# Optimization experiments

Measured on AMD Instinct MI355X. Metric: run time of the kernel, lower is better.

The kernel has to match this reference:

```python
import jax, jax.numpy as jnp
import numpy as np

TEMPERATURE = 0.07
MARGIN = 0.2
EPS = 1e-8  # matches torch F.cosine_similarity eps


def _cosine_matrix(a, b):
    # a: (N, D), b: (M, D) -> (N, M) pairwise cosine similarity
    an = a / jnp.clip(jnp.linalg.norm(a, axis=-1, keepdims=True), EPS)
    bn = b / jnp.clip(jnp.linalg.norm(b, axis=-1, keepdims=True), EPS)
    return an @ bn.T


def setup_inputs() -> dict:
    key = jax.random.key(0)
    k1, k2, k3 = jax.random.split(key, 3)
    return {
        "step_embeddings": jax.random.normal(k1, (8192, 1024), dtype=jnp.float32),
        "modal_embeddings": jax.random.normal(k2, (4096, 1024), dtype=jnp.float32),
        "negative_modal_embeddings": jax.random.normal(k3, (4096, 1024), dtype=jnp.float32),
    }


def reference(step_embeddings, modal_embeddings, negative_modal_embeddings):
    # --- step-modal alignment (max cosine sim per step, averaged) ---
    S = _cosine_matrix(step_embeddings, modal_embeddings)        # (N, M)
    per_step = S.max(axis=1)                                      # (N,)
    alignment = per_step.mean()

    # --- attention-weighted alignment (use_attention=True) ---
    logits = (step_embeddings @ modal_embeddings.T) / TEMPERATURE  # (N, M)
    attention = jax.nn.softmax(logits, axis=1)
    weighted_alignment = (S * attention).sum(axis=1).mean()

    # --- contrastive coherence against negatives ---
    Sn = _cosine_matrix(step_embeddings, negative_modal_embeddings)
    negative_alignment = Sn.max(axis=1).mean()
    positive_alignment = alignment
    contrastive_score = positive_alignment - negative_alignment
    margin_score = jax.nn.relu(contrastive_score - MARGIN)

    # --- per-step coherence (same max-cosine per step) ---
    min_step_coherence = per_step.min()

    # overall uses weighted_alignment (attention on), mixed with contrastive
    overall = 0.7 * weighted_alignment + 0.3 * contrastive_score

    return (alignment, weighted_alignment, attention, contrastive_score,
            margin_score, positive_alignment, negative_alignment,
            per_step, min_step_coherence, overall)
```

## Files before the change

### kernel.cpp

```cpp
#include <hip/hip_runtime.h>
#include <cmath>


#define WAVE 64

typedef __bf16 bf16x8_t __attribute__((ext_vector_type(8)));
typedef __bf16 bf16x4_t __attribute__((ext_vector_type(4)));
typedef float f32x4_t __attribute__((ext_vector_type(4)));

__device__ __forceinline__ float wave_reduce_sum(float v) {
#pragma unroll
    for (int o = 32; o > 0; o >>= 1) v += __shfl_down(v, o, WAVE);
    return v;
}
__device__ __forceinline__ float wave_reduce_max(float v) {
#pragma unroll
    for (int o = 32; o > 0; o >>= 1) v = fmaxf(v, __shfl_down(v, o, WAVE));
    return v;
}
__device__ __forceinline__ float wave_reduce_min(float v) {
#pragma unroll
    for (int o = 32; o > 0; o >>= 1) v = fminf(v, __shfl_down(v, o, WAVE));
    return v;
}

__device__ __forceinline__ unsigned enc_f(float f) {
    unsigned u = __float_as_uint(f);
    return (u & 0x80000000u) ? ~u : (u | 0x80000000u);
}
__device__ __forceinline__ float dec_f(unsigned e) {
    unsigned u = (e & 0x80000000u) ? (e & 0x7fffffffu) : ~e;
    return __uint_as_float(u);
}

__global__ __launch_bounds__(256)
void convert_norms_kernel(const float* __restrict__ step,
                          const float* __restrict__ modal,
                          const float* __restrict__ negs,
                          char* __restrict__ arena,
                          float* __restrict__ ina, float* __restrict__ inb,
                          float* __restrict__ inn,
                          unsigned* __restrict__ negmax_u, int N, int M) {
    const int tid = threadIdx.x, lane = tid & 63, wv = tid >> 6;
    const int b = blockIdx.x * 4 + wv;
    const float* src;
    if (b < N)          src = step  + (size_t)b * 1024;
    else if (b < N + M) src = modal + (size_t)(b - N) * 1024;
    else                src = negs  + (size_t)(b - N - M) * 1024;

    char* cb = arena + (((size_t)(b >> 2)) << 14) + ((size_t)(b & 3) << 11) + 8192;
    float s = 0.0f;
#pragma unroll
    for (int q = 0; q < 4; q++) {
        const int idx = lane + q * 64;
        const float4 v = ((const float4*)src)[idx];
        bf16x4_t o;
        o[0] = (__bf16)v.x; o[1] = (__bf16)v.y;
        o[2] = (__bf16)v.z; o[3] = (__bf16)v.w;
        *(bf16x4_t*)(cb + (size_t)idx * 8) = o;
        s += v.x * v.x + v.y * v.y + v.z * v.z + v.w * v.w;
    }
    s = wave_reduce_sum(s);
    if (lane == 0) {
        const float inv = 1.0f / fmaxf(sqrtf(s), 1e-8f);
        if (b < N)          { ina[b] = inv; negmax_u[b] = 0u; }
        else if (b < N + M) inb[b - N] = inv;
        else                inn[b - N - M] = inv;
    }
}

#define GLD16(g, l)                                                        \
    __builtin_amdgcn_global_load_lds(                                     \
        (const __attribute__((address_space(1))) void*)(g),               \
        (__attribute__((address_space(3))) void*)(l), 16, 0, 0)

#define PIPE_BARRIER() asm volatile(                                       \
    "s_waitcnt vmcnt(0) lgkmcnt(0)\n\ts_barrier" ::: "memory")

__global__ __launch_bounds__(256, 2)
void gemm_fused_kernel(char* __restrict__ arena, int N, int M,
                       const float* __restrict__ inv_nn,
                       unsigned* __restrict__ negmax_u) {
    __shared__ __bf16 As[2][128 * 64];
    __shared__ __bf16 Bs[2][128 * 64];

    const int lin = blockIdx.x;
    const int st  = lin >> 7;
    const int r128 = lin & 127;
    const int bxi = (st & 7) * 8 + (r128 & 7);
    const int byi = (st >> 3) * 16 + (r128 >> 3);
    const int bm = byi * 128, bn = bxi * 128;

    const int t = threadIdx.x, w = t >> 6, lane = t & 63;
    const int lane16 = lane & 15, lq = lane >> 4;
    const int wm = (w & 1) * 64, wn = (w >> 1) * 64;

    const int s_is_b  = w >> 1;
    const int rowbase = (w & 1) * 64;
    const int ln3 = lane >> 3;
    const int q_g = (lane & 7) ^ ln3;
    const int cbase = (s_is_b ? (N + bn) : bm) + rowbase;
    const int cc = cbase + ln3;
    const size_t off0 = (((size_t)(cc >> 2)) << 14) +
                        ((size_t)(cc & 3) << 11) + 8192 + (size_t)q_g * 16;
    const char* gbase = arena + off0;
    const int ldsoff = rowbase * 64;
    __bf16* ldsw0 = (s_is_b ? Bs[0] : As[0]) + ldsoff;
    __bf16* ldsw1 = (s_is_b ? Bs[1] : As[1]) + ldsoff;

    f32x4_t acc[4][4];
#pragma unroll
    for (int i = 0; i < 4; i++)
#pragma unroll
        for (int j = 0; j < 4; j++) acc[i][j] = (f32x4_t){0.f, 0.f, 0.f, 0.f};

    const int sxr = lane16 & 7;

#pragma unroll
    for (int r = 0; r < 8; r++)
        GLD16(gbase + (size_t)r * 32768, ldsw0 + r * 512);

    for (int it = 0; it < 16; ++it) {
        PIPE_BARRIER();
        const int cur = it & 1;

        bf16x8_t af[2][4], bf[2][4];
#pragma unroll
        for (int kk = 0; kk < 2; kk++) {
            const int qo = ((lq + kk * 4) ^ sxr) * 8;
#pragma unroll
            for (int i = 0; i < 4; i++)
                af[kk][i] = *(const bf16x8_t*)&As[cur][(wm + i * 16 + lane16) * 64 + qo];
#pragma unroll
            for (int j = 0; j < 4; j++)
                bf[kk][j] = *(const bf16x8_t*)&Bs[cur][(wn + j * 16 + lane16) * 64 + qo];
        }

        if (it + 1 < 16) {
            const size_t k0b = (size_t)(it + 1) * 128;
            __bf16* ldsw = cur ? ldsw0 : ldsw1;
#pragma unroll
            for (int r = 0; r < 8; r++)
                GLD16(gbase + (size_t)r * 32768 + k0b, ldsw + r * 512);
        }

#pragma unroll
        for (int kk = 0; kk < 2; kk++)
#pragma unroll
            for (int i = 0; i < 4; i++)
#pragma unroll
                for (int j = 0; j < 4; j++)
                    acc[i][j] = __builtin_amdgcn_mfma_f32_16x16x32_bf16(
                        af[kk][i], bf[kk][j], acc[i][j], 0, 0, 0);
    }

    if (bn < M) {
#pragma unroll
        for (int i = 0; i < 4; i++) {
#pragma unroll
            for (int r = 0; r < 4; r++) {
                const int grow = bm + wm + i * 16 + lq * 4 + r;
                __bf16* dst = (__bf16*)(arena + ((size_t)grow << 14)) +
                              bn + wn + lane16;
#pragma unroll
                for (int j = 0; j < 4; j++)
                    dst[j * 16] = (__bf16)acc[i][j][r];
            }
        }
    } else {
        float invn[4];
#pragma unroll
        for (int j = 0; j < 4; j++)
            invn[j] = inv_nn[(bn - M) + wn + j * 16 + lane16];
#pragma unroll
        for (int i = 0; i < 4; i++) {
#pragma unroll
            for (int r = 0; r < 4; r++) {
                float v = acc[i][0][r] * invn[0];
                v = fmaxf(v, acc[i][1][r] * invn[1]);
                v = fmaxf(v, acc[i][2][r] * invn[2]);
                v = fmaxf(v, acc[i][3][r] * invn[3]);
#pragma unroll
                for (int o = 8; o > 0; o >>= 1)
                    v = fmaxf(v, __shfl_xor(v, o, WAVE));
                if (lane16 == 0)
                    atomicMax(&negmax_u[bm + wm + i * 16 + lq * 4 + r], enc_f(v));
            }
        }
    }
}

#define CUT 2.0f
#define MAXCAND 64

__global__ __launch_bounds__(256)
void softmax_fix_kernel(char* __restrict__ arena, const float* __restrict__ step,
                        const float* __restrict__ modal,
                        const float* __restrict__ ina, const float* __restrict__ inb,
                        float* __restrict__ perstep, float* __restrict__ wout,
                        float* __restrict__ attn) {
    const int row = blockIdx.x, tid = threadIdx.x;
    const int lane = tid & 63, wv = tid >> 6;

    __shared__ float srow_s[1024];
    __shared__ float red[8];
    __shared__ float bcast[2];
    __shared__ int   cand[MAXCAND];
    __shared__ float exact[MAXCAND];
    __shared__ int   cnt;

    if (tid == 0) cnt = 0;
    ((float4*)srow_s)[tid] = ((const float4*)(step + (size_t)row * 1024))[tid];

    const __bf16* gb = (const __bf16*)(arena + ((size_t)row << 14));
    float vals[16];
    float invn[16];
#pragma unroll
    for (int g = 0; g < 4; g++) {
        const bf16x4_t v = *(const bf16x4_t*)(gb + g * 1024 + tid * 4);
        const float4 x = *(const float4*)(inb + g * 1024 + tid * 4);
        vals[g * 4 + 0] = (float)v[0]; vals[g * 4 + 1] = (float)v[1];
        vals[g * 4 + 2] = (float)v[2]; vals[g * 4 + 3] = (float)v[3];
        invn[g * 4 + 0] = x.x; invn[g * 4 + 1] = x.y;
        invn[g * 4 + 2] = x.z; invn[g * 4 + 3] = x.w;
    }

    float dmax = -3.4e38f;
#pragma unroll
    for (int j = 0; j < 16; j++) dmax = fmaxf(dmax, vals[j]);
    float wm = wave_reduce_max(dmax);
    if (lane == 0) red[wv] = wm;
    __syncthreads();
    if (tid == 0) bcast[0] = fmaxf(fmaxf(red[0], red[1]), fmaxf(red[2], red[3]));
    __syncthreads();
    const float m0 = bcast[0];

    const float thr = m0 - CUT;
#pragma unroll
    for (int g = 0; g < 4; g++)
#pragma unroll
        for (int u = 0; u < 4; u++) {
            if (vals[g * 4 + u] >= thr) {
                const int pos = atomicAdd(&cnt, 1);
                if (pos < MAXCAND) cand[pos] = g * 1024 + tid * 4 + u;
            }
        }
    __syncthreads();
    const int nc = min(cnt, MAXCAND);

    for (int i = wv; i < nc; i += 4) {
        const float* mrow = modal + (size_t)cand[i] * 1024;
        float p = 0.0f;
#pragma unroll
        for (int q = 0; q < 16; q++) {
            const int idx = lane + q * 64;
            p = fmaf(srow_s[idx], mrow[idx], p);
        }
        p = wave_reduce_sum(p);
        if (lane == 0) exact[i] = p;
    }
    __syncthreads();

    for (int i = 0; i < nc; i++) {
        const int c = cand[i];
        if (((c & 1023) >> 2) == tid) vals[(c >> 10) * 4 + (c & 3)] = exact[i];
    }

    float dmax2 = -3.4e38f, cmax = -3.4e38f;
#pragma unroll
    for (int j = 0; j < 16; j++) {
        dmax2 = fmaxf(dmax2, vals[j]);
        cmax = fmaxf(cmax, vals[j] * invn[j]);
    }
    float wg = wave_reduce_max(dmax2);
    float wc = wave_reduce_max(cmax);
    if (lane == 0) { red[wv] = wg; red[4 + wv] = wc; }
    __syncthreads();
    if (tid == 0) {
        bcast[0] = fmaxf(fmaxf(red[0], red[1]), fmaxf(red[2], red[3]));
        bcast[1] = fmaxf(fmaxf(red[4], red[5]), fmaxf(red[6], red[7]));
    }
    __syncthreads();
    const float invT = 1.0f / 0.07f;
    const float mlog = bcast[0] * invT;
    const float cmaxAll = bcast[1];

    float evals[16];
    float lsum = 0.0f;
#pragma unroll
    for (int j = 0; j < 16; j++) {
        const float e = __expf(vals[j] * invT - mlog);
        evals[j] = e;
        lsum += e;
    }
    lsum = wave_reduce_sum(lsum);
    __syncthreads();
    if (lane == 0) red[wv] = lsum;
    __syncthreads();
    if (tid == 0) bcast[0] = red[0] + red[1] + red[2] + red[3];
    __syncthreads();
    const float invZ = 1.0f / bcast[0];

    float* arow = attn + (size_t)row * 4096;
    float wacc = 0.0f;
#pragma unroll
    for (int g = 0; g < 4; g++) {
        float4 o;
        const float a0 = evals[g * 4 + 0] * invZ, a1 = evals[g * 4 + 1] * invZ;
        const float a2 = evals[g * 4 + 2] * invZ, a3 = evals[g * 4 + 3] * invZ;
        o.x = a0; o.y = a1; o.z = a2; o.w = a3;
        *(float4*)(arow + g * 1024 + tid * 4) = o;
        wacc += a0 * vals[g * 4 + 0] * invn[g * 4 + 0];
        wacc += a1 * vals[g * 4 + 1] * invn[g * 4 + 1];
        wacc += a2 * vals[g * 4 + 2] * invn[g * 4 + 2];
        wacc += a3 * vals[g * 4 + 3] * invn[g * 4 + 3];
    }
    wacc = wave_reduce_sum(wacc);
    __syncthreads();
    if (lane == 0) red[wv] = wacc;
    __syncthreads();
    if (tid == 0) {
        const float inv_na = ina[row];
        perstep[row] = cmaxAll * inv_na;
        wout[row] = (red[0] + red[1] + red[2] + red[3]) * inv_na;
    }
}

__global__ __launch_bounds__(1024)
void finalize_kernel(const float* __restrict__ perstep, const float* __restrict__ w,
                     const unsigned* __restrict__ negmax_u,
                     const float* __restrict__ ina, float* __restrict__ out,
                     int N, size_t NM) {
    float s_a = 0.0f, s_w = 0.0f, s_n = 0.0f, mn = 3.4e38f;
    for (int i = threadIdx.x; i < N; i += 1024) {
        const float p = perstep[i];
        s_a += p;
        s_w += w[i];
        s_n += dec_f(negmax_u[i]) * ina[i];
        mn = fminf(mn, p);
    }
    s_a = wave_reduce_sum(s_a);
    s_w = wave_reduce_sum(s_w);
    s_n = wave_reduce_sum(s_n);
    mn  = wave_reduce_min(mn);
    __shared__ float ra[16], rw[16], rn[16], rm[16];
    const int lane = threadIdx.x & 63, wv = threadIdx.x >> 6;
    if (lane == 0) { ra[wv] = s_a; rw[wv] = s_w; rn[wv] = s_n; rm[wv] = mn; }
    __syncthreads();
    if (threadIdx.x == 0) {
        float ta = 0, tw = 0, tn = 0, tm = 3.4e38f;
#pragma unroll
        for (int i = 0; i < 16; i++) {
            ta += ra[i]; tw += rw[i]; tn += rn[i]; tm = fminf(tm, rm[i]);
        }
        const float inv = 1.0f / (float)N;
        const float alignment = ta * inv;
        const float weighted  = tw * inv;
        const float neg       = tn * inv;
        const float contrast  = alignment - neg;
        const float margin    = fmaxf(contrast - 0.2f, 0.0f);
        const float overall   = 0.7f * weighted + 0.3f * contrast;
        out[0] = alignment;
        out[1] = weighted;
        float* p = out + 2 + NM;
        p[0] = contrast;
        p[1] = margin;
        p[2] = alignment;
        p[3] = neg;
        p[4 + N] = tm;
        p[5 + N] = overall;
    }
}

extern "C" void kernel_launch(void* const* d_in, const int* in_sizes, int n_in,
                              void* d_out, int out_size, void* d_ws, size_t ws_size,
                              hipStream_t stream) {
    const float* step  = (const float*)d_in[0];
    const float* modal = (const float*)d_in[1];
    const float* negs  = (const float*)d_in[2];
    float* out = (float*)d_out;

    const int K = 1024;
    const int N = in_sizes[0] / K;
    const int M = in_sizes[1] / K;
    const size_t NM = (size_t)N * (size_t)M;

    float* ina        = (float*)d_ws;
    float* inb        = ina + N;
    float* inn        = inb + M;
    unsigned* negmax  = (unsigned*)(inn + M);
    float* wsum       = (float*)(negmax + N);

    char* arena    = (char*)d_out + 16;
    float* attn    = out + 2;
    float* perstep = out + 2 + NM + 4;

    convert_norms_kernel<<<(N + 2 * M) / 4, 256, 0, stream>>>(
        step, modal, negs, arena, ina, inb, inn, negmax, N, M);

    const int nblocks = (N / 128) * ((2 * M) / 128);
    gemm_fused_kernel<<<nblocks, 256, 0, stream>>>(arena, N, M, inn, negmax);

    softmax_fix_kernel<<<N, 256, 0, stream>>>(arena, step, modal, ina, inb,
                                              perstep, wsum, attn);

    finalize_kernel<<<1, 1024, 0, stream>>>(perstep, wsum, negmax, ina, out, N, NM);
}
```

Measured before the change: 398.9 us.

## Switch GEMM mainloop to triple-buffered K=32 stages with partial vmcnt waits

Replaces the double-buffered K=64 LDS pipeline with three smaller K=32 stages. Each iteration prefetches two stages ahead and waits only on older loads (vmcnt(4)) rather than draining all outstanding global loads. LDS per block drops from 64 KB to 48 KB, and launch bounds rise to 3 blocks per CU to increase occupancy. The cost is twice as many barriers per tile, less MFMA work between barriers, and tighter register pressure at the higher occupancy target.

```diff
diff --git a/kernel.cpp b/kernel.cpp
--- a/kernel.cpp
+++ b/kernel.cpp
@@ -69,20 +69,17 @@
     }
 }
 
-#define GLD16(g, l)                                                        \
+#define GLD16(g, l)                                                       \
     __builtin_amdgcn_global_load_lds(                                     \
         (const __attribute__((address_space(1))) void*)(g),               \
         (__attribute__((address_space(3))) void*)(l), 16, 0, 0)
 
-#define PIPE_BARRIER() asm volatile(                                       \
-    "s_waitcnt vmcnt(0) lgkmcnt(0)\n\ts_barrier" ::: "memory")
-
-__global__ __launch_bounds__(256, 2)
+__global__ __launch_bounds__(256, 3)
 void gemm_fused_kernel(char* __restrict__ arena, int N, int M,
                        const float* __restrict__ inv_nn,
                        unsigned* __restrict__ negmax_u) {
-    __shared__ __bf16 As[2][128 * 64];
-    __shared__ __bf16 Bs[2][128 * 64];
+    __shared__ __bf16 smA[3][128 * 32];
+    __shared__ __bf16 smB[3][128 * 32];
 
     const int lin = blockIdx.x;
     const int st  = lin >> 7;
@@ -95,18 +92,19 @@
     const int lane16 = lane & 15, lq = lane >> 4;
     const int wm = (w & 1) * 64, wn = (w >> 1) * 64;
 
-    const int s_is_b  = w >> 1;
-    const int rowbase = (w & 1) * 64;
-    const int ln3 = lane >> 3;
-    const int q_g = (lane & 7) ^ ln3;
-    const int cbase = (s_is_b ? (N + bn) : bm) + rowbase;
-    const int cc = cbase + ln3;
-    const size_t off0 = (((size_t)(cc >> 2)) << 14) +
-                        ((size_t)(cc & 3) << 11) + 8192 + (size_t)q_g * 16;
-    const char* gbase = arena + off0;
-    const int ldsoff = rowbase * 64;
-    __bf16* ldsw0 = (s_is_b ? Bs[0] : As[0]) + ldsoff;
-    __bf16* ldsw1 = (s_is_b ? Bs[1] : As[1]) + ldsoff;
+    const int s_is_b = w >> 1;
+    const int wrow   = (w & 1) * 64;
+    const int rl = lane >> 2, ql = lane & 3;
+    const int o_sw = ql ^ ((rl >> 1) & 3);
+    const int cbase = (s_is_b ? (N + bn) : bm) + wrow;
+
+    const char* ga[4];
+#pragma unroll
+    for (int g = 0; g < 4; g++) {
+        const int c = cbase + g * 16 + rl;
+        ga[g] = arena + (((size_t)(c >> 2)) << 14) + ((size_t)(c & 3) << 11)
+                + 8192 + (size_t)o_sw * 16;
+    }
 
     f32x4_t acc[4][4];
 #pragma unroll
@@ -114,44 +112,52 @@
 #pragma unroll
         for (int j = 0; j < 4; j++) acc[i][j] = (f32x4_t){0.f, 0.f, 0.f, 0.f};
 
-    const int sxr = lane16 & 7;
-
-#pragma unroll
-    for (int r = 0; r < 8; r++)
-        GLD16(gbase + (size_t)r * 32768, ldsw0 + r * 512);
-
-    for (int it = 0; it < 16; ++it) {
-        PIPE_BARRIER();
-        const int cur = it & 1;
-
-        bf16x8_t af[2][4], bf[2][4];
-#pragma unroll
-        for (int kk = 0; kk < 2; kk++) {
-            const int qo = ((lq + kk * 4) ^ sxr) * 8;
-#pragma unroll
-            for (int i = 0; i < 4; i++)
-                af[kk][i] = *(const bf16x8_t*)&As[cur][(wm + i * 16 + lane16) * 64 + qo];
+    const int fsw = (lane16 >> 1) & 3;
+    const int a_base = (wm + lane16) * 32 + (lq ^ fsw) * 8;
+    const int b_base = (wn + lane16) * 32 + (lq ^ fsw) * 8;
+
+#pragma unroll
+    for (int g = 0; g < 4; g++) {
+        __bf16* d0 = (s_is_b ? smB[0] : smA[0]) + wrow * 32 + g * 512;
+        GLD16(ga[g], d0);
+    }
+#pragma unroll
+    for (int g = 0; g < 4; g++) {
+        __bf16* d1 = (s_is_b ? smB[1] : smA[1]) + wrow * 32 + g * 512;
+        GLD16(ga[g] + 64, d1);
+    }
+
+#pragma unroll
+    for (int it = 0; it < 32; ++it) {
+        if (it < 31)
+            asm volatile("s_waitcnt vmcnt(4) lgkmcnt(0)\n\ts_barrier" ::: "memory");
+        else
+            asm volatile("s_waitcnt vmcnt(0) lgkmcnt(0)\n\ts_barrier" ::: "memory");
+
+        const int cur = it % 3;
+
+        if (it < 30) {
+            const int nx = (it + 2) % 3;
+            __bf16* d = (s_is_b ? smB[nx] : smA[nx]) + wrow * 32;
+#pragma unroll
+            for (int g = 0; g < 4; g++)
+                GLD16(ga[g] + (it + 2) * 64, d + g * 512);
+        }
+
+        bf16x8_t af[4], bf[4];
+#pragma unroll
+        for (int i = 0; i < 4; i++)
+            af[i] = *(const bf16x8_t*)&smA[cur][a_base + i * 512];
+#pragma unroll
+        for (int j = 0; j < 4; j++)
+            bf[j] = *(const bf16x8_t*)&smB[cur][b_base + j * 512];
+
+#pragma unroll
+        for (int i = 0; i < 4; i++)
 #pragma unroll
             for (int j = 0; j < 4; j++)
-                bf[kk][j] = *(const bf16x8_t*)&Bs[cur][(wn + j * 16 + lane16) * 64 + qo];
-        }
-
-        if (it + 1 < 16) {
-            const size_t k0b = (size_t)(it + 1) * 128;
-            __bf16* ldsw = cur ? ldsw0 : ldsw1;
-#pragma unroll
-            for (int r = 0; r < 8; r++)
-                GLD16(gbase + (size_t)r * 32768 + k0b, ldsw + r * 512);
-        }
-
-#pragma unroll
-        for (int kk = 0; kk < 2; kk++)
-#pragma unroll
-            for (int i = 0; i < 4; i++)
-#pragma unroll
-                for (int j = 0; j < 4; j++)
-                    acc[i][j] = __builtin_amdgcn_mfma_f32_16x16x32_bf16(
-                        af[kk][i], bf[kk][j], acc[i][j], 0, 0, 0);
+                acc[i][j] = __builtin_amdgcn_mfma_f32_16x16x32_bf16(
+                    af[i], bf[j], acc[i][j], 0, 0, 0);
     }
 
     if (bn < M) {
```

After: 434.5 us. 1.09x slower.

## Fuse row max and candidate selection into GEMM epilogue, drop dot-matrix round trip

Applied to the files above, without the earlier changes.

The GEMM epilogue no longer writes the bf16 step-modal dot matrix. It computes per-row dot and cosine maxima with atomics and records near-max candidate columns in a small per-row list. A new resolve kernel recomputes the candidates exactly in fp32 and builds a sparse softmax, writing zeros for all other attention entries. Rows whose candidate list overflows fall back to a slow full fp32 recomputation. This removes a large intermediate write and read, but truncates the softmax to at most 16 terms and adds atomic contention in the epilogue.

```diff
diff --git a/kernel.cpp b/kernel.cpp
--- a/kernel.cpp
+++ b/kernel.cpp
@@ -3,6 +3,8 @@
 
 
 #define WAVE 64
+#define CUT 2.0f
+#define CAP 64
 
 typedef __bf16 bf16x8_t __attribute__((ext_vector_type(8)));
 typedef __bf16 bf16x4_t __attribute__((ext_vector_type(4)));
@@ -40,7 +42,10 @@
                           char* __restrict__ arena,
                           float* __restrict__ ina, float* __restrict__ inb,
                           float* __restrict__ inn,
-                          unsigned* __restrict__ negmax_u, int N, int M) {
+                          unsigned* __restrict__ negmax_u,
+                          unsigned* __restrict__ dotmax_u,
+                          unsigned* __restrict__ cosmax_u,
+                          int* __restrict__ cnt, int N, int M) {
     const int tid = threadIdx.x, lane = tid & 63, wv = tid >> 6;
     const int b = blockIdx.x * 4 + wv;
     const float* src;
@@ -48,7 +53,7 @@
     else if (b < N + M) src = modal + (size_t)(b - N) * 1024;
     else                src = negs  + (size_t)(b - N - M) * 1024;
 
-    char* cb = arena + (((size_t)(b >> 2)) << 14) + ((size_t)(b & 3) << 11) + 8192;
+    char* cb = arena + (size_t)b * 2048;
     float s = 0.0f;
 #pragma unroll
     for (int q = 0; q < 4; q++) {
@@ -63,24 +68,32 @@
     s = wave_reduce_sum(s);
     if (lane == 0) {
         const float inv = 1.0f / fmaxf(sqrtf(s), 1e-8f);
-        if (b < N)          { ina[b] = inv; negmax_u[b] = 0u; }
-        else if (b < N + M) inb[b - N] = inv;
-        else                inn[b - N - M] = inv;
-    }
-}
-
-#define GLD16(g, l)                                                        \
+        if (b < N) {
+            ina[b] = inv;
+            negmax_u[b] = 0u; dotmax_u[b] = 0u; cosmax_u[b] = 0u; cnt[b] = 0;
+        } else if (b < N + M) inb[b - N] = inv;
+        else                  inn[b - N - M] = inv;
+    }
+}
+
+#define GLD16(g, l)                                                       \
     __builtin_amdgcn_global_load_lds(                                     \
         (const __attribute__((address_space(1))) void*)(g),               \
         (__attribute__((address_space(3))) void*)(l), 16, 0, 0)
 
-#define PIPE_BARRIER() asm volatile(                                       \
+#define PIPE_BARRIER() asm volatile(                                      \
     "s_waitcnt vmcnt(0) lgkmcnt(0)\n\ts_barrier" ::: "memory")
 
 __global__ __launch_bounds__(256, 2)
-void gemm_fused_kernel(char* __restrict__ arena, int N, int M,
+void gemm_fused_kernel(const char* __restrict__ arena, int N, int M,
+                       const float* __restrict__ inv_nb,
                        const float* __restrict__ inv_nn,
-                       unsigned* __restrict__ negmax_u) {
+                       unsigned* __restrict__ negmax_u,
+                       unsigned* __restrict__ dotmax_u,
+                       unsigned* __restrict__ cosmax_u,
+                       int* __restrict__ cnt,
+                       int* __restrict__ candcol,
+                       float* __restrict__ canddot) {
     __shared__ __bf16 As[2][128 * 64];
     __shared__ __bf16 Bs[2][128 * 64];
 
@@ -100,10 +113,7 @@
     const int ln3 = lane >> 3;
     const int q_g = (lane & 7) ^ ln3;
     const int cbase = (s_is_b ? (N + bn) : bm) + rowbase;
-    const int cc = cbase + ln3;
-    const size_t off0 = (((size_t)(cc >> 2)) << 14) +
-                        ((size_t)(cc & 3) << 11) + 8192 + (size_t)q_g * 16;
-    const char* gbase = arena + off0;
+    const char* gbase = arena + (size_t)(cbase + ln3) * 2048 + (size_t)q_g * 16;
     const int ldsoff = rowbase * 64;
     __bf16* ldsw0 = (s_is_b ? Bs[0] : As[0]) + ldsoff;
     __bf16* ldsw1 = (s_is_b ? Bs[1] : As[1]) + ldsoff;
@@ -118,7 +128,7 @@
 
 #pragma unroll
     for (int r = 0; r < 8; r++)
-        GLD16(gbase + (size_t)r * 32768, ldsw0 + r * 512);
+        GLD16(gbase + (size_t)r * 16384, ldsw0 + r * 512);
 
     for (int it = 0; it < 16; ++it) {
         PIPE_BARRIER();
@@ -141,7 +151,7 @@
             __bf16* ldsw = cur ? ldsw0 : ldsw1;
 #pragma unroll
             for (int r = 0; r < 8; r++)
-                GLD16(gbase + (size_t)r * 32768 + k0b, ldsw + r * 512);
+                GLD16(gbase + (size_t)r * 16384 + k0b, ldsw + r * 512);
         }
 
 #pragma unroll
@@ -155,16 +165,43 @@
     }
 
     if (bn < M) {
+        float invnj[4];
+#pragma unroll
+        for (int j = 0; j < 4; j++)
+            invnj[j] = inv_nb[bn + wn + j * 16 + lane16];
 #pragma unroll
         for (int i = 0; i < 4; i++) {
 #pragma unroll
             for (int r = 0; r < 4; r++) {
-                const int grow = bm + wm + i * 16 + lq * 4 + r;
-                __bf16* dst = (__bf16*)(arena + ((size_t)grow << 14)) +
-                              bn + wn + lane16;
-#pragma unroll
-                for (int j = 0; j < 4; j++)
-                    dst[j * 16] = (__bf16)acc[i][j][r];
+                const int row = bm + wm + i * 16 + lq * 4 + r;
+                float d0 = acc[i][0][r], d1 = acc[i][1][r];
+                float d2 = acc[i][2][r], d3 = acc[i][3][r];
+                float dm = fmaxf(fmaxf(d0, d1), fmaxf(d2, d3));
+                float cm = fmaxf(fmaxf(d0 * invnj[0], d1 * invnj[1]),
+                                 fmaxf(d2 * invnj[2], d3 * invnj[3]));
+#pragma unroll
+                for (int o = 8; o > 0; o >>= 1) {
+                    dm = fmaxf(dm, __shfl_xor(dm, o, WAVE));
+                    cm = fmaxf(cm, __shfl_xor(cm, o, WAVE));
+                }
+                unsigned old = 0u;
+                if (lane16 == 0) {
+                    old = atomicMax(&dotmax_u[row], enc_f(dm));
+                    atomicMax(&cosmax_u[row], enc_f(cm));
+                }
+                old = __shfl(old, lane & 48, WAVE);
+                const float thr = fmaxf(dec_f(old), dm) - CUT;
+                float dj[4] = {d0, d1, d2, d3};
+#pragma unroll
+                for (int j = 0; j < 4; j++) {
+                    if (dj[j] >= thr) {
+                        const int pos = atomicAdd(&cnt[row], 1);
+                        if (pos < CAP) {
+                            candcol[row * CAP + pos] = bn + wn + j * 16 + lane16;
+                            canddot[row * CAP + pos] = dj[j];
+                        }
+                    }
+                }
             }
         }
     } else {
@@ -190,139 +227,138 @@
     }
 }
 
-#define CUT 2.0f
-#define MAXCAND 64
-
 __global__ __launch_bounds__(256)
-void softmax_fix_kernel(char* __restrict__ arena, const float* __restrict__ step,
-                        const float* __restrict__ modal,
-                        const float* __restrict__ ina, const float* __restrict__ inb,
-                        float* __restrict__ perstep, float* __restrict__ wout,
-                        float* __restrict__ attn) {
+void resolve_kernel(const float* __restrict__ step, const float* __restrict__ modal,
+                    const float* __restrict__ ina, const float* __restrict__ inb,
+                    const unsigned* __restrict__ cosmax_u,
+                    const int* __restrict__ cnt,
+                    const int* __restrict__ candcol,
+                    const float* __restrict__ canddot,
+                    float* __restrict__ perstep, float* __restrict__ wsum,
+                    float* __restrict__ attn) {
     const int row = blockIdx.x, tid = threadIdx.x;
     const int lane = tid & 63, wv = tid >> 6;
 
-    __shared__ float srow_s[1024];
-    __shared__ float red[8];
-    __shared__ float bcast[2];
-    __shared__ int   cand[MAXCAND];
-    __shared__ float exact[MAXCAND];
-    __shared__ int   cnt;
-
-    if (tid == 0) cnt = 0;
-    ((float4*)srow_s)[tid] = ((const float4*)(step + (size_t)row * 1024))[tid];
-
-    const __bf16* gb = (const __bf16*)(arena + ((size_t)row << 14));
-    float vals[16];
-    float invn[16];
-#pragma unroll
-    for (int g = 0; g < 4; g++) {
-        const bf16x4_t v = *(const bf16x4_t*)(gb + g * 1024 + tid * 4);
-        const float4 x = *(const float4*)(inb + g * 1024 + tid * 4);
-        vals[g * 4 + 0] = (float)v[0]; vals[g * 4 + 1] = (float)v[1];
-        vals[g * 4 + 2] = (float)v[2]; vals[g * 4 + 3] = (float)v[3];
-        invn[g * 4 + 0] = x.x; invn[g * 4 + 1] = x.y;
-        invn[g * 4 + 2] = x.z; invn[g * 4 + 3] = x.w;
-    }
-
-    float dmax = -3.4e38f;
-#pragma unroll
-    for (int j = 0; j < 16; j++) dmax = fmaxf(dmax, vals[j]);
-    float wm = wave_reduce_max(dmax);
-    if (lane == 0) red[wv] = wm;
+    __shared__ float srow[1024];
+    __shared__ float dots[4096];
+    __shared__ int   lcol[CAP];
+    __shared__ float ldot[CAP];
+    __shared__ int   flist[16];
+    __shared__ float fattn[16];
+    __shared__ float fexact[16];
+    __shared__ int   fn_s;
+    __shared__ float red8[8];
+    __shared__ float sc[2];
+
+    ((float4*)srow)[tid] = ((const float4*)(step + (size_t)row * 1024))[tid];
+
+    const int rawcnt = cnt[row];
+    const int nc = min(rawcnt, CAP);
+    if (tid < nc) {
+        lcol[tid] = candcol[row * CAP + tid];
+        ldot[tid] = canddot[row * CAP + tid];
+    }
     __syncthreads();
-    if (tid == 0) bcast[0] = fmaxf(fmaxf(red[0], red[1]), fmaxf(red[2], red[3]));
-    __syncthreads();
-    const float m0 = bcast[0];
-
-    const float thr = m0 - CUT;
-#pragma unroll
-    for (int g = 0; g < 4; g++)
-#pragma unroll
-        for (int u = 0; u < 4; u++) {
-            if (vals[g * 4 + u] >= thr) {
-                const int pos = atomicAdd(&cnt, 1);
-                if (pos < MAXCAND) cand[pos] = g * 1024 + tid * 4 + u;
+
+    const float invT = 1.0f / 0.07f;
+    float* arow = attn + (size_t)row * 4096;
+
+    if (rawcnt <= CAP) {
+        if (tid == 0) {
+            float m0 = -3.4e38f; int am = 0;
+            for (int i = 0; i < nc; i++)
+                if (ldot[i] > m0) { m0 = ldot[i]; am = i; }
+            int fn = 0;
+            flist[fn++] = lcol[am];
+            const float thr = m0 - CUT;
+            for (int i = 0; i < nc && fn < 16; i++)
+                if (i != am && ldot[i] >= thr) flist[fn++] = lcol[i];
+            fn_s = fn;
+        }
+        __syncthreads();
+        const int fn = fn_s;
+
+        for (int i = wv; i < fn; i += 4) {
+            const float* mrow = modal + (size_t)flist[i] * 1024;
+            float p = 0.0f;
+#pragma unroll
+            for (int q = 0; q < 16; q++) {
+                const int idx = lane + q * 64;
+                p = fmaf(srow[idx], mrow[idx], p);
             }
-        }
-    __syncthreads();
-    const int nc = min(cnt, MAXCAND);
-
-    for (int i = wv; i < nc; i += 4) {
-        const float* mrow = modal + (size_t)cand[i] * 1024;
-        float p = 0.0f;
-#pragma unroll
-        for (int q = 0; q < 16; q++) {
-            const int idx = lane + q * 64;
-            p = fmaf(srow_s[idx], mrow[idx], p);
-        }
-        p = wave_reduce_sum(p);
-        if (lane == 0) exact[i] = p;
-    }
-    __syncthreads();
-
-    for (int i = 0; i < nc; i++) {
-        const int c = cand[i];
-        if (((c & 1023) >> 2) == tid) vals[(c >> 10) * 4 + (c & 3)] = exact[i];
-    }
-
-    float dmax2 = -3.4e38f, cmax = -3.4e38f;
-#pragma unroll
-    for (int j = 0; j < 16; j++) {
-        dmax2 = fmaxf(dmax2, vals[j]);
-        cmax = fmaxf(cmax, vals[j] * invn[j]);
-    }
-    float wg = wave_reduce_max(dmax2);
-    float wc = wave_reduce_max(cmax);
-    if (lane == 0) { red[wv] = wg; red[4 + wv] = wc; }
-    __syncthreads();
-    if (tid == 0) {
-        bcast[0] = fmaxf(fmaxf(red[0], red[1]), fmaxf(red[2], red[3]));
-        bcast[1] = fmaxf(fmaxf(red[4], red[5]), fmaxf(red[6], red[7]));
-    }
-    __syncthreads();
-    const float invT = 1.0f / 0.07f;
-    const float mlog = bcast[0] * invT;
-    const float cmaxAll = bcast[1];
-
-    float evals[16];
-    float lsum = 0.0f;
-#pragma unroll
-    for (int j = 0; j < 16; j++) {
-        const float e = __expf(vals[j] * invT - mlog);
-        evals[j] = e;
-        lsum += e;
-    }
-    lsum = wave_reduce_sum(lsum);
-    __syncthreads();
-    if (lane == 0) red[wv] = lsum;
-    __syncthreads();
-    if (tid == 0) bcast[0] = red[0] + red[1] + red[2] + red[3];
-    __syncthreads();
-    const float invZ = 1.0f / bcast[0];
-
-    float* arow = attn + (size_t)row * 4096;
-    float wacc = 0.0f;
-#pragma unroll
-    for (int g = 0; g < 4; g++) {
-        float4 o;
-        const float a0 = evals[g * 4 + 0] * invZ, a1 = evals[g * 4 + 1] * invZ;
-        const float a2 = evals[g * 4 + 2] * invZ, a3 = evals[g * 4 + 3] * invZ;
-        o.x = a0; o.y = a1; o.z = a2; o.w = a3;
-        *(float4*)(arow + g * 1024 + tid * 4) = o;
-        wacc += a0 * vals[g * 4 + 0] * invn[g * 4 + 0];
-        wacc += a1 * vals[g * 4 + 1] * invn[g * 4 + 1];
-        wacc += a2 * vals[g * 4 + 2] * invn[g * 4 + 2];
-        wacc += a3 * vals[g * 4 + 3] * invn[g * 4 + 3];
-    }
-    wacc = wave_reduce_sum(wacc);
-    __syncthreads();
-    if (lane == 0) red[wv] = wacc;
-    __syncthreads();
-    if (tid == 0) {
-        const float inv_na = ina[row];
-        perstep[row] = cmaxAll * inv_na;
-        wout[row] = (red[0] + red[1] + red[2] + red[3]) * inv_na;
+            p = wave_reduce_sum(p);
+            if (lane == 0) fexact[i] = p;
+        }
+        __syncthreads();
+
+        if (tid == 0) {
+            float m = -3.4e38f;
+            for (int i = 0; i < fn; i++) m = fmaxf(m, fexact[i]);
+            float Z = 0.0f;
+            for (int i = 0; i < fn; i++) Z += __expf((fexact[i] - m) * invT);
+            const float invZ = 1.0f / Z;
+            float wacc = 0.0f;
+            for (int i = 0; i < fn; i++) {
+                const float a = __expf((fexact[i] - m) * invT) * invZ;
+                fattn[i] = a;
+                wacc += a * fexact[i] * inb[flist[i]];
+            }
+            const float ia = ina[row];
+            wsum[row] = wacc * ia;
+            perstep[row] = dec_f(cosmax_u[row]) * ia;
+        }
+        __syncthreads();
+
+#pragma unroll
+        for (int g = 0; g < 4; g++) {
+            const int c0 = g * 1024 + tid * 4;
+            float4 o = {0.f, 0.f, 0.f, 0.f};
+            for (int i = 0; i < fn; i++) {
+                const int d = flist[i] - c0;
+                if ((unsigned)d < 4u) ((float*)&o)[d] = fattn[i];
+            }
+            *(float4*)(arow + c0) = o;
+        }
+    } else {
+        for (int c = tid; c < 4096; c += 256) {
+            const float* mrow = modal + (size_t)c * 1024;
+            float p = 0.0f;
+            for (int k = 0; k < 1024; k++) p = fmaf(srow[k], mrow[k], p);
+            dots[c] = p;
+        }
+        __syncthreads();
+        float m = -3.4e38f;
+        for (int c = tid; c < 4096; c += 256) m = fmaxf(m, dots[c]);
+        m = wave_reduce_max(m);
+        if (lane == 0) red8[wv] = m;
+        __syncthreads();
+        if (tid == 0) sc[0] = fmaxf(fmaxf(red8[0], red8[1]), fmaxf(red8[2], red8[3]));
+        __syncthreads();
+        m = sc[0];
+        float Zp = 0.0f;
+        for (int c = tid; c < 4096; c += 256) Zp += __expf((dots[c] - m) * invT);
+        Zp = wave_reduce_sum(Zp);
+        __syncthreads();
+        if (lane == 0) red8[wv] = Zp;
+        __syncthreads();
+        if (tid == 0) sc[1] = red8[0] + red8[1] + red8[2] + red8[3];
+        __syncthreads();
+        const float invZ = 1.0f / sc[1];
+        float wacc = 0.0f;
+        for (int c = tid; c < 4096; c += 256) {
+            const float a = __expf((dots[c] - m) * invT) * invZ;
+            arow[c] = a;
+            wacc += a * dots[c] * inb[c];
+        }
+        wacc = wave_reduce_sum(wacc);
+        __syncthreads();
+        if (lane == 0) red8[wv] = wacc;
+        __syncthreads();
+        if (tid == 0) {
+            const float ia = ina[row];
+            wsum[row] = (red8[0] + red8[1] + red8[2] + red8[3]) * ia;
+            perstep[row] = dec_f(cosmax_u[row]) * ia;
+        }
     }
 }
 
@@ -385,24 +421,33 @@
     const int M = in_sizes[1] / K;
     const size_t NM = (size_t)N * (size_t)M;
 
-    float* ina        = (float*)d_ws;
-    float* inb        = ina + N;
-    float* inn        = inb + M;
-    unsigned* negmax  = (unsigned*)(inn + M);
-    float* wsum       = (float*)(negmax + N);
+    float*    ina      = (float*)d_ws;
+    float*    inb      = ina + N;
+    float*    inn      = inb + M;
+    unsigned* negmax_u = (unsigned*)(inn + M);
+    unsigned* dotmax_u = negmax_u + N;
+    unsigned* cosmax_u = dotmax_u + N;
+    int*      cnt      = (int*)(cosmax_u + N);
+    float*    wsum     = (float*)(cnt + N);
+    int*      candcol  = (int*)(wsum + N);
+    float*    canddot  = (float*)(candcol + (size_t)N * CAP);
 
     char* arena    = (char*)d_out + 16;
     float* attn    = out + 2;
     float* perstep = out + 2 + NM + 4;
 
     convert_norms_kernel<<<(N + 2 * M) / 4, 256, 0, stream>>>(
-        step, modal, negs, arena, ina, inb, inn, negmax, N, M);
+        step, modal, negs, arena, ina, inb, inn,
+        negmax_u, dotmax_u, cosmax_u, cnt, N, M);
 
     const int nblocks = (N / 128) * ((2 * M) / 128);
-    gemm_fused_kernel<<<nblocks, 256, 0, stream>>>(arena, N, M, inn, negmax);
-
-    softmax_fix_kernel<<<N, 256, 0, stream>>>(arena, step, modal, ina, inb,
-                                              perstep, wsum, attn);
-
-    finalize_kernel<<<1, 1024, 0, stream>>>(perstep, wsum, negmax, ina, out, N, NM);
-}
+    gemm_fused_kernel<<<nblocks, 256, 0, stream>>>(
+        arena, N, M, inb, inn, negmax_u, dotmax_u, cosmax_u,
+        cnt, candcol, canddot);
+
+    resolve_kernel<<<N, 256, 0, stream>>>(
+        step, modal, ina, inb, cosmax_u, cnt, candcol, canddot,
+        perstep, wsum, attn);
+
+    finalize_kernel<<<1, 1024, 0, stream>>>(perstep, wsum, negmax_u, ina, out, N, NM);
+}
```

After: 449.8 us. 12.8% more time.
